# Performance work log

Hardware: AMD Instinct MI355X
Metric: run time of the kernel (lower is better)

The kernel has to match this reference:

```python
import jax, jax.numpy as jnp
import numpy as np

N_ITEMS = 100000
K_IL = 64

def setup_inputs() -> dict:
    key = jax.random.key(0)
    k1, k2, k3 = jax.random.split(key, 3)
    X = jax.random.randint(k1, (1024, 10, 4), 0, N_ITEMS, dtype=jnp.int64)
    IL = jax.random.normal(k2, (N_ITEMS, K_IL), dtype=jnp.float32)
    LI = jax.random.normal(k3, (N_ITEMS, K_IL), dtype=jnp.float32)
    return {"X": X, "IL": IL, "LI": LI, "tag": 0}

def reference(X, IL, LI, tag):
    # tag==0 path: score every item for each row's previous item.
    # predictions[b, i] = sum_k IL[i, k] * LI[prev[b], k] / sqrt(k_IL)
    prev = X[:, -2, 3]                       # [B] previous item ids
    li_prev = LI[prev]                       # [B, K] gather
    scale = 1.0 / (IL.shape[1] ** 0.5)
    return jnp.einsum('bk,ik->bi', li_prev, IL) * scale  # [B, N_ITEMS]
```

## Files before the change

### kernel.cpp

```cpp
#include <hip/hip_runtime.h>
#include <hip/hip_bf16.h>


typedef short short8 __attribute__((ext_vector_type(8)));
typedef float f32x4 __attribute__((ext_vector_type(4)));
typedef unsigned short ushort4v __attribute__((ext_vector_type(4)));

#define KDIM 64
#define LDSS 72

static __device__ __forceinline__ unsigned short f2bf(float f) {
    unsigned u = __float_as_uint(f);
    unsigned r = (u + 0x7fffu + ((u >> 16) & 1u)) >> 16;
    return (unsigned short)r;
}

__global__ __launch_bounds__(256)
void fpmc_gemm(const int* __restrict__ X,
               const float* __restrict__ IL,
               const float* __restrict__ LI,
               float* __restrict__ out,
               int M, int N) {
    __shared__ unsigned short As[128 * LDSS];
    __shared__ unsigned short Bs[128 * LDSS];

    const int t  = threadIdx.x;
    const int m0 = blockIdx.y * 128;
    const int i0 = blockIdx.x * 128;

    {
        const int rb = t >> 4;
        const int c  = (t & 15) * 4;
        #pragma unroll
        for (int it = 0; it < 8; ++it) {
            const int r = it * 16 + rb;
            const int idx = X[(m0 + r) * 40 + 35];
            const float4 v = *(const float4*)(LI + (size_t)idx * KDIM + c);
            ushort4v p;
            p.x = f2bf(v.x); p.y = f2bf(v.y); p.z = f2bf(v.z); p.w = f2bf(v.w);
            *(ushort4v*)&As[r * LDSS + c] = p;
        }
    }
    {
        const int rb = t >> 4;
        const int c  = (t & 15) * 4;
        #pragma unroll
        for (int it = 0; it < 8; ++it) {
            const int r = it * 16 + rb;
            int gi = i0 + r;
            if (gi > N - 1) gi = N - 1;
            const float4 v = *(const float4*)(IL + (size_t)gi * KDIM + c);
            ushort4v p;
            p.x = f2bf(v.x); p.y = f2bf(v.y); p.z = f2bf(v.z); p.w = f2bf(v.w);
            *(ushort4v*)&Bs[r * LDSS + c] = p;
        }
    }
    __syncthreads();

    const int w    = t >> 6;
    const int l    = t & 63;
    const int row  = l & 15;
    const int quad = l >> 4;
    const int mw   = (w & 1) * 64;
    const int nw   = (w >> 1) * 64;

    f32x4 acc[4][4];
    #pragma unroll
    for (int mt = 0; mt < 4; ++mt)
        #pragma unroll
        for (int nt = 0; nt < 4; ++nt)
            acc[mt][nt] = (f32x4){0.f, 0.f, 0.f, 0.f};

    #pragma unroll
    for (int ks = 0; ks < KDIM; ks += 32) {
        short8 a[4], b[4];
        #pragma unroll
        for (int mt = 0; mt < 4; ++mt)
            a[mt] = *(const short8*)&As[(mw + mt * 16 + row) * LDSS + ks + quad * 8];
        #pragma unroll
        for (int nt = 0; nt < 4; ++nt)
            b[nt] = *(const short8*)&Bs[(nw + nt * 16 + row) * LDSS + ks + quad * 8];
        #pragma unroll
        for (int mt = 0; mt < 4; ++mt)
            #pragma unroll
            for (int nt = 0; nt < 4; ++nt)
                acc[mt][nt] = __builtin_amdgcn_mfma_f32_16x16x32_bf16(
                    a[mt], b[nt], acc[mt][nt], 0, 0, 0);
    }

    const float scale = 0.125f;
    #pragma unroll
    for (int mt = 0; mt < 4; ++mt) {
        #pragma unroll
        for (int reg = 0; reg < 4; ++reg) {
            const int m = m0 + mw + mt * 16 + quad * 4 + reg;
            float* orow = out + (size_t)m * N;
            #pragma unroll
            for (int nt = 0; nt < 4; ++nt) {
                const int n = i0 + nw + nt * 16 + row;
                if (n < N) orow[n] = acc[mt][nt][reg] * scale;
            }
        }
    }
}

extern "C" void kernel_launch(void* const* d_in, const int* in_sizes, int n_in,
                              void* d_out, int out_size, void* d_ws, size_t ws_size,
                              hipStream_t stream) {
    const int*   X  = (const int*)d_in[0];
    const float* IL = (const float*)d_in[1];
    const float* LI = (const float*)d_in[2];
    float* out = (float*)d_out;

    const int M = in_sizes[0] / 40;
    const int N = in_sizes[1] / KDIM;

    dim3 grid((N + 127) / 128, M / 128);
    fpmc_gemm<<<grid, dim3(256), 0, stream>>>(X, IL, LI, out, M, N);
}
```

Baseline: 513.1 us.

## Stage output tile through LDS for 16-byte nontemporal row stores

Swaps the MFMA operand order so each lane holds four consecutive columns, then stages accumulator tiles through padded shared memory and writes the output as 16-byte vector nontemporal stores along rows instead of scattered 4-byte stores. The output matrix is large and write-bandwidth bound, so wider coalesced stores that bypass cache should cut store traffic overhead. It adds extra LDS round trips and barriers in the epilogue. The n<N guard on vector stores assumes N is a multiple of 4, which holds here.

```diff
diff --git a/kernel.cpp b/kernel.cpp
--- a/kernel.cpp
+++ b/kernel.cpp
@@ -1,5 +1,4 @@
 #include <hip/hip_runtime.h>
-#include <hip/hip_bf16.h>
 
 
 typedef short short8 __attribute__((ext_vector_type(8)));
@@ -8,6 +7,7 @@
 
 #define KDIM 64
 #define LDSS 72
+#define EPS  68
 
 static __device__ __forceinline__ unsigned short f2bf(float f) {
     unsigned u = __float_as_uint(f);
@@ -21,8 +21,9 @@
                const float* __restrict__ LI,
                float* __restrict__ out,
                int M, int N) {
-    __shared__ unsigned short As[128 * LDSS];
-    __shared__ unsigned short Bs[128 * LDSS];
+    __shared__ __align__(16) unsigned short SMEM[2 * 128 * LDSS];
+    unsigned short* As = SMEM;
+    unsigned short* Bs = SMEM + 128 * LDSS;
 
     const int t  = threadIdx.x;
     const int m0 = blockIdx.y * 128;
@@ -85,20 +86,37 @@
             #pragma unroll
             for (int nt = 0; nt < 4; ++nt)
                 acc[mt][nt] = __builtin_amdgcn_mfma_f32_16x16x32_bf16(
-                    a[mt], b[nt], acc[mt][nt], 0, 0, 0);
+                    b[nt], a[mt], acc[mt][nt], 0, 0, 0);
     }
 
+    float* T = reinterpret_cast<float*>(SMEM);
     const float scale = 0.125f;
+
     #pragma unroll
-    for (int mt = 0; mt < 4; ++mt) {
+    for (int mb = 0; mb < 4; mb += 2) {
+        __syncthreads();
         #pragma unroll
-        for (int reg = 0; reg < 4; ++reg) {
-            const int m = m0 + mw + mt * 16 + quad * 4 + reg;
-            float* orow = out + (size_t)m * N;
+        for (int s = 0; s < 2; ++s) {
+            float* Tw = T + (w * 2 + s) * (16 * EPS);
             #pragma unroll
             for (int nt = 0; nt < 4; ++nt) {
-                const int n = i0 + nw + nt * 16 + row;
-                if (n < N) orow[n] = acc[mt][nt][reg] * scale;
+                f32x4 v = acc[mb + s][nt] * scale;
+                *(f32x4*)&Tw[row * EPS + nt * 16 + quad * 4] = v;
+            }
+        }
+        __syncthreads();
+        #pragma unroll
+        for (int s = 0; s < 2; ++s) {
+            const float* Tw = T + (w * 2 + s) * (16 * EPS);
+            const int gm = m0 + mw + (mb + s) * 16;
+            const int n  = i0 + nw + row * 4;
+            #pragma unroll
+            for (int p = 0; p < 4; ++p) {
+                const int ml = p * 4 + quad;
+                f32x4 v = *(const f32x4*)&Tw[ml * EPS + row * 4];
+                if (n < N)
+                    __builtin_nontemporal_store(
+                        v, (f32x4*)(out + (size_t)(gm + ml) * N + n));
             }
         }
     }
```

Measured after the change: 506.4 us. No clear change (-1.3%).

## Pre-gather LI rows to bf16 workspace and stream IL directly into MFMA

Applied to the files above, without the earlier changes.

Adds a separate gather kernel that converts the indexed LI rows to bf16 once into workspace. The GEMM now uses 256x256 slabs with only the A slab kept in LDS. IL rows are loaded from global memory straight into registers for each 32-column chunk. Operands are swapped so each lane holds four contiguous output columns, written with vectorized nontemporal stores. This targets the strided scalar output writes and the repeated per-block LI gather and conversion, but IL is now read without LDS staging and an extra kernel launch is added.

```diff
diff --git a/kernel.cpp b/kernel.cpp
--- a/kernel.cpp
+++ b/kernel.cpp
@@ -1,38 +1,68 @@
 #include <hip/hip_runtime.h>
-#include <hip/hip_bf16.h>
 
 
 typedef short short8 __attribute__((ext_vector_type(8)));
 typedef float f32x4 __attribute__((ext_vector_type(4)));
 typedef unsigned short ushort4v __attribute__((ext_vector_type(4)));
+typedef unsigned short ushort8v __attribute__((ext_vector_type(8)));
 
-#define KDIM 64
-#define LDSS 72
+#define KDIM  64
+#define LDSS  72
+#define MSLAB 256
+#define NSLAB 256
+#define NCH   32
 
 static __device__ __forceinline__ unsigned short f2bf(float f) {
     unsigned u = __float_as_uint(f);
-    unsigned r = (u + 0x7fffu + ((u >> 16) & 1u)) >> 16;
-    return (unsigned short)r;
+    return (unsigned short)((u + 0x7fffu + ((u >> 16) & 1u)) >> 16);
+}
+
+static __device__ __forceinline__ short8 cvt8(float4 v0, float4 v1) {
+    union { ushort8v u; short8 s; } r;
+    r.u[0] = f2bf(v0.x); r.u[1] = f2bf(v0.y); r.u[2] = f2bf(v0.z); r.u[3] = f2bf(v0.w);
+    r.u[4] = f2bf(v1.x); r.u[5] = f2bf(v1.y); r.u[6] = f2bf(v1.z); r.u[7] = f2bf(v1.w);
+    return r.s;
 }
 
 __global__ __launch_bounds__(256)
-void fpmc_gemm(const int* __restrict__ X,
-               const float* __restrict__ IL,
-               const float* __restrict__ LI,
-               float* __restrict__ out,
-               int M, int N) {
-    __shared__ unsigned short As[128 * LDSS];
-    __shared__ unsigned short Bs[128 * LDSS];
+void fpmc_gather(const int* __restrict__ X, const float* __restrict__ LI,
+                 unsigned short* __restrict__ ws, int M) {
+    const int t = threadIdx.x;
+    const int r = blockIdx.x * 16 + (t >> 4);
+    if (r >= M) return;
+    const int c = (t & 15) * 4;
+    const int idx = X[r * 40 + 35];
+    const float4 v = *(const float4*)(LI + (size_t)idx * KDIM + c);
+    ushort4v p;
+    p.x = f2bf(v.x); p.y = f2bf(v.y); p.z = f2bf(v.z); p.w = f2bf(v.w);
+    *(ushort4v*)(ws + (size_t)r * KDIM + c) = p;
+}
+
+template<bool USE_WS>
+__global__ __launch_bounds__(256, 4)
+void fpmc_gemm2(const int* __restrict__ X, const float* __restrict__ IL,
+                const float* __restrict__ LI, const unsigned short* __restrict__ Aws,
+                float* __restrict__ out, int M, int N) {
+    __shared__ __align__(16) unsigned short As[MSLAB * LDSS];
 
     const int t  = threadIdx.x;
-    const int m0 = blockIdx.y * 128;
-    const int i0 = blockIdx.x * 128;
+    const int m0 = blockIdx.y * MSLAB;
+    const int i0 = blockIdx.x * NSLAB;
 
-    {
+    if (USE_WS) {
+        #pragma unroll
+        for (int it = 0; it < 8; ++it) {
+            const int chunk = it * 256 + t;
+            const int r = chunk >> 3;
+            const int c = (chunk & 7) * 8;
+            ushort8v v = *(const ushort8v*)(Aws + (size_t)(m0 + r) * KDIM + c);
+            *(ushort8v*)&As[r * LDSS + c] = v;
+        }
+    } else {
         const int rb = t >> 4;
         const int c  = (t & 15) * 4;
         #pragma unroll
-        for (int it = 0; it < 8; ++it) {
+        for (int it = 0; it < MSLAB / 16; ++it) {
             const int r = it * 16 + rb;
             const int idx = X[(m0 + r) * 40 + 35];
             const float4 v = *(const float4*)(LI + (size_t)idx * KDIM + c);
@@ -41,64 +71,59 @@
             *(ushort4v*)&As[r * LDSS + c] = p;
         }
     }
-    {
-        const int rb = t >> 4;
-        const int c  = (t & 15) * 4;
-        #pragma unroll
-        for (int it = 0; it < 8; ++it) {
-            const int r = it * 16 + rb;
-            int gi = i0 + r;
-            if (gi > N - 1) gi = N - 1;
-            const float4 v = *(const float4*)(IL + (size_t)gi * KDIM + c);
-            ushort4v p;
-            p.x = f2bf(v.x); p.y = f2bf(v.y); p.z = f2bf(v.z); p.w = f2bf(v.w);
-            *(ushort4v*)&Bs[r * LDSS + c] = p;
-        }
-    }
     __syncthreads();
 
     const int w    = t >> 6;
     const int l    = t & 63;
-    const int row  = l & 15;
+    const int lr   = l & 15;
     const int quad = l >> 4;
-    const int mw   = (w & 1) * 64;
-    const int nw   = (w >> 1) * 64;
+    const int mwav = w * 64;
+    const float scale = 0.125f;
 
-    f32x4 acc[4][4];
-    #pragma unroll
-    for (int mt = 0; mt < 4; ++mt)
-        #pragma unroll
-        for (int nt = 0; nt < 4; ++nt)
-            acc[mt][nt] = (f32x4){0.f, 0.f, 0.f, 0.f};
+    for (int nc = 0; nc < NSLAB / NCH; ++nc) {
+        const int n0c = i0 + nc * NCH;
 
-    #pragma unroll
-    for (int ks = 0; ks < KDIM; ks += 32) {
-        short8 a[4], b[4];
-        #pragma unroll
-        for (int mt = 0; mt < 4; ++mt)
-            a[mt] = *(const short8*)&As[(mw + mt * 16 + row) * LDSS + ks + quad * 8];
-        #pragma unroll
-        for (int nt = 0; nt < 4; ++nt)
-            b[nt] = *(const short8*)&Bs[(nw + nt * 16 + row) * LDSS + ks + quad * 8];
+        f32x4 acc[4][2];
         #pragma unroll
         for (int mt = 0; mt < 4; ++mt)
             #pragma unroll
-            for (int nt = 0; nt < 4; ++nt)
-                acc[mt][nt] = __builtin_amdgcn_mfma_f32_16x16x32_bf16(
-                    a[mt], b[nt], acc[mt][nt], 0, 0, 0);
-    }
+            for (int nt = 0; nt < 2; ++nt)
+                acc[mt][nt] = (f32x4){0.f, 0.f, 0.f, 0.f};
 
-    const float scale = 0.125f;
-    #pragma unroll
-    for (int mt = 0; mt < 4; ++mt) {
         #pragma unroll
-        for (int reg = 0; reg < 4; ++reg) {
-            const int m = m0 + mw + mt * 16 + quad * 4 + reg;
+        for (int ks = 0; ks < 2; ++ks) {
+            short8 b[2];
+            #pragma unroll
+            for (int nt = 0; nt < 2; ++nt) {
+                int n = n0c + nt * 16 + lr;
+                if (n > N - 1) n = N - 1;
+                const float* p = IL + (size_t)n * KDIM + ks * 32 + quad * 8;
+                b[nt] = cvt8(*(const float4*)p, *(const float4*)(p + 4));
+            }
+            short8 a[4];
+            #pragma unroll
+            for (int mt = 0; mt < 4; ++mt)
+                a[mt] = *(const short8*)&As[(mwav + mt * 16 + lr) * LDSS + ks * 32 + quad * 8];
+            #pragma unroll
+            for (int mt = 0; mt < 4; ++mt)
+                #pragma unroll
+                for (int nt = 0; nt < 2; ++nt)
+                    acc[mt][nt] = __builtin_amdgcn_mfma_f32_16x16x32_bf16(
+                        b[nt], a[mt], acc[mt][nt], 0, 0, 0);
+        }
+
+        #pragma unroll
+        for (int mt = 0; mt < 4; ++mt) {
+            const int m = m0 + mwav + mt * 16 + lr;
+            if (m >= M) continue;
             float* orow = out + (size_t)m * N;
             #pragma unroll
-            for (int nt = 0; nt < 4; ++nt) {
-                const int n = i0 + nw + nt * 16 + row;
-                if (n < N) orow[n] = acc[mt][nt][reg] * scale;
+            for (int nt = 0; nt < 2; ++nt) {
+                const int n = n0c + nt * 16 + quad * 4;
+                if (n < N) {
+                    f32x4 v = acc[mt][nt] * scale;
+                    __builtin_nontemporal_store(v, (f32x4*)(orow + n));
+                }
             }
         }
     }
@@ -115,6 +140,14 @@
     const int M = in_sizes[0] / 40;
     const int N = in_sizes[1] / KDIM;
 
-    dim3 grid((N + 127) / 128, M / 128);
-    fpmc_gemm<<<grid, dim3(256), 0, stream>>>(X, IL, LI, out, M, N);
+    unsigned short* Aws = (unsigned short*)d_ws;
+    const size_t need = (size_t)M * KDIM * sizeof(unsigned short);
+
+    dim3 grid((N + NSLAB - 1) / NSLAB, (M + MSLAB - 1) / MSLAB);
+    if (d_ws != nullptr && ws_size >= need) {
+        fpmc_gather<<<dim3((M + 15) / 16), dim3(256), 0, stream>>>(X, LI, Aws, M);
+        fpmc_gemm2<true><<<grid, dim3(256), 0, stream>>>(X, IL, LI, Aws, out, M, N);
+    } else {
+        fpmc_gemm2<false><<<grid, dim3(256), 0, stream>>>(X, IL, LI, Aws, out, M, N);
+    }
 }
```

Result: faster. 484.1 us (-5.7%).
